# Kernel optimization log

Hardware: AMD Instinct MI355X
Metric: run time of the kernel (lower is better)

The kernel has to match this reference:

```python
import jax, jax.numpy as jnp
import numpy as np

N_SRC, N_DST, E = 50000, 50000, 800000
D_GT, D_AG = 64, 64
HID, HEADS = 256, 4
FPH = HID // HEADS  # 64
N_ACT = 16
NEG_SLOPE = 0.2  # DGL GATv2Conv default negative_slope


def setup_inputs() -> dict:
    key = jax.random.key(0)
    ks = jax.random.split(key, 16)
    f32 = jnp.float32
    return {
        "feat_gt": jax.random.normal(ks[0], (N_SRC, D_GT), f32),
        "feat_agent": jax.random.normal(ks[1], (N_DST, D_AG), f32),
        "h0": jax.random.normal(ks[2], (N_DST, HID), f32),
        "edge_src": jax.random.randint(ks[3], (E,), 0, N_SRC),
        "edge_dst": jax.random.randint(ks[4], (E,), 0, N_DST),
        "W_src": jax.random.normal(ks[5], (D_GT, HID), f32) * 0.1,
        "b_src": jnp.zeros((HID,), f32),
        "W_dst": jax.random.normal(ks[6], (D_AG, HID), f32) * 0.1,
        "b_dst": jnp.zeros((HID,), f32),
        "attn": jax.random.normal(ks[7], (HEADS, FPH), f32) * 0.1,
        "W_res": jax.random.normal(ks[8], (D_AG, HID), f32) * 0.1,
        "b_res": jnp.zeros((HID,), f32),
        "W_ih": jax.random.normal(ks[9], (3 * HID, HID), f32) * 0.05,
        "W_hh": jax.random.normal(ks[10], (3 * HID, HID), f32) * 0.05,
        "b_ih": jnp.zeros((3 * HID,), f32),
        "b_hh": jnp.zeros((3 * HID,), f32),
        "W_out": jax.random.normal(ks[11], (HID, N_ACT), f32) * 0.05,
        "b_out": jnp.zeros((N_ACT,), f32),
    }


def _gatv2(feat_gt, feat_agent, edge_src, edge_dst,
           W_src, b_src, W_dst, b_dst, attn, W_res, b_res):
    # GATv2Conv (bipartite, share_weights=False, residual=True, activation=ReLU)
    fs = (feat_gt @ W_src + b_src).reshape(N_SRC, HEADS, FPH)    # [Ns,H,F]
    fd = (feat_agent @ W_dst + b_dst).reshape(N_DST, HEADS, FPH)  # [Nd,H,F]
    e = fs[edge_src] + fd[edge_dst]                               # [E,H,F]
    e = jnp.where(e > 0, e, NEG_SLOPE * e)                        # LeakyReLU
    score = jnp.einsum('ehf,hf->eh', e, attn)                     # [E,H]
    # edge softmax segmented by destination node
    smax = jax.lax.stop_gradient(
        jax.ops.segment_max(score, edge_dst, num_segments=N_DST))  # [Nd,H]
    ex = jnp.exp(score - smax[edge_dst])
    den = jax.ops.segment_sum(ex, edge_dst, num_segments=N_DST)   # [Nd,H]
    alpha = ex / den[edge_dst]                                    # [E,H]
    msg = alpha[:, :, None] * fs[edge_src]                        # [E,H,F]
    rst = jax.ops.segment_sum(msg, edge_dst, num_segments=N_DST)  # [Nd,H,F]
    rst = rst.reshape(N_DST, HID) + (feat_agent @ W_res + b_res)  # residual
    return jax.nn.relu(rst)


def _gru_cell(x, h, W_ih, W_hh, b_ih, b_hh):
    gi = x @ W_ih.T + b_ih
    gh = h @ W_hh.T + b_hh
    ir, iz, inn = jnp.split(gi, 3, axis=-1)
    hr, hz, hn = jnp.split(gh, 3, axis=-1)
    r = jax.nn.sigmoid(ir + hr)
    z = jax.nn.sigmoid(iz + hz)
    n = jnp.tanh(inn + r * hn)
    return (1.0 - z) * n + z * h


def reference(feat_gt, feat_agent, h0, edge_src, edge_dst,
              W_src, b_src, W_dst, b_dst, attn, W_res, b_res,
              W_ih, W_hh, b_ih, b_hh, W_out, b_out):
    x = _gatv2(feat_gt, feat_agent, edge_src, edge_dst,
               W_src, b_src, W_dst, b_dst, attn, W_res, b_res)  # [Nd,HID]
    h = _gru_cell(x, h0, W_ih, W_hh, b_ih, b_hh)                # [Nd,HID]
    logits = h @ W_out + b_out                                  # [Nd,N_ACT]
    return (logits, h)
```

## Files before the change

kernel.cpp:

```cpp
#include <hip/hip_runtime.h>
#include <stdint.h>

#define N_SRCN 50000
#define N_DSTN 50000
#define NE     800000
#define HIDN   256
#define NEG    0.2f

typedef __attribute__((ext_vector_type(8)))  short short8;
typedef __attribute__((ext_vector_type(16))) float float16v;

__device__ __forceinline__ float bf2f(unsigned short u){
    union { unsigned u32; float f; } c; c.u32 = ((unsigned)u) << 16; return c.f;
}
__device__ __forceinline__ unsigned short f2bf(float f){
    union { float f; unsigned u; } c; c.f = f;
    unsigned r = c.u + 0x7fffu + ((c.u >> 16) & 1u);
    return (unsigned short)(r >> 16);
}
__device__ __forceinline__ float4 ld4b(const unsigned short* p){
    uint2 u = *reinterpret_cast<const uint2*>(p);
    float4 r;
    r.x = bf2f((unsigned short)(u.x & 0xffff));
    r.y = bf2f((unsigned short)(u.x >> 16));
    r.z = bf2f((unsigned short)(u.y & 0xffff));
    r.w = bf2f((unsigned short)(u.y >> 16));
    return r;
}
__device__ __forceinline__ void gload_lds16(const unsigned short* g, unsigned short* l){
    __builtin_amdgcn_global_load_lds(
        (const __attribute__((address_space(1))) void*)g,
        (__attribute__((address_space(3))) void*)l,
        16, 0, 0);
}

__global__ void pack_kernel(const float* __restrict__ Wsrc, const float* __restrict__ Wdst,
                            const float* __restrict__ Wres, const float* __restrict__ Wih,
                            const float* __restrict__ Whh,
                            unsigned short* __restrict__ Wt2,
                            unsigned short* __restrict__ Wf){
    int i = blockIdx.x * 256 + threadIdx.x;
    if (i < 49152){
        int which = i >> 14, j = i & 16383;
        int k = j >> 8, c = j & 255;
        const float* W = (which == 0) ? Wsrc : (which == 1 ? Wdst : Wres);
        float v = W[j];
        int off = which * 16384 + (c >> 5) * 2048 + (k >> 4) * 512
                + (((k >> 3) & 1) * 32 + (c & 31)) * 8 + (k & 7);
        Wt2[off] = f2bf(v);
    } else if (i < 49152 + 196608){
        int o = i - 49152;
        int row = o >> 8, k = o & 255;
        int g = row >> 8, c = row & 255;
        float v = Wih[o];
        int off = g * 131072 + (c >> 5) * 16384 + (k >> 4) * 512
                + (((k >> 3) & 1) * 32 + (c & 31)) * 8 + (k & 7);
        Wf[off] = f2bf(v);
    } else if (i < 49152 + 393216){
        int o = i - 49152 - 196608;
        int row = o >> 8, k = o & 255;
        int g = row >> 8, c = row & 255;
        float v = Whh[o];
        int off = g * 131072 + (c >> 5) * 16384 + (16 + (k >> 4)) * 512
                + (((k >> 3) & 1) * 32 + (c & 31)) * 8 + (k & 7);
        Wf[off] = f2bf(v);
    }
}

__global__ __launch_bounds__(256) void proj_kernel(
        const float* __restrict__ Agt, const float* __restrict__ Aag,
        const unsigned short* __restrict__ Wt2,
        const float* __restrict__ bsrc, const float* __restrict__ bdst,
        const float* __restrict__ bres,
        unsigned short* __restrict__ fs, unsigned short* __restrict__ fd,
        unsigned short* __restrict__ resb){
    __shared__ unsigned short As[64 * 72];
    __shared__ unsigned short Cs[64 * 72];
    int z = blockIdx.z;
    const float* A = (z == 0) ? Agt : Aag;
    const float* bias = (z == 0) ? bsrc : (z == 1 ? bdst : bres);
    unsigned short* out = (z == 0) ? fs : (z == 1 ? fd : resb);
    const unsigned short* Wb = Wt2 + z * 16384;
    int tid = threadIdx.x;
    int m0 = blockIdx.y * 64;
    #pragma unroll
    for (int i = 0; i < 4; ++i){
        int ci = tid + i * 256;
        int row = ci >> 4;
        int k4 = (ci & 15) << 2;
        int gr = m0 + row; if (gr >= N_SRCN) gr = N_SRCN - 1;
        float4 v = *reinterpret_cast<const float4*>(A + (size_t)gr * 64 + k4);
        unsigned short* dp = As + row * 72 + k4;
        dp[0] = f2bf(v.x); dp[1] = f2bf(v.y); dp[2] = f2bf(v.z); dp[3] = f2bf(v.w);
    }
    __syncthreads();
    int lane = tid & 63, w = tid >> 6;
    int l31 = lane & 31, half = lane >> 5;
    int msub = (w & 1) * 32;
    int cbw = blockIdx.x * 2 + (w >> 1);
    const unsigned short* bb = Wb + cbw * 2048 + lane * 8;
    const unsigned short* ap = As + (msub + l31) * 72 + half * 8;
    float16v acc = {0,0,0,0,0,0,0,0,0,0,0,0,0,0,0,0};
    #pragma unroll
    for (int ks = 0; ks < 4; ++ks){
        short8 a = *reinterpret_cast<const short8*>(ap + ks * 16);
        short8 b = *reinterpret_cast<const short8*>(bb + ks * 512);
        acc = __builtin_amdgcn_mfma_f32_32x32x16_bf16(a, b, acc, 0, 0, 0);
    }
    float bv = bias[cbw * 32 + l31];
    int ccol = (w >> 1) * 32 + l31;
    #pragma unroll
    for (int r = 0; r < 16; ++r){
        int row = (r & 3) + 8 * (r >> 2) + 4 * half + msub;
        Cs[row * 72 + ccol] = f2bf(acc[r] + bv);
    }
    __syncthreads();
    int srow = tid >> 2, chunk = tid & 3;
    int gr2 = m0 + srow;
    if (gr2 < N_SRCN){
        const uint4* sp = reinterpret_cast<const uint4*>(Cs + srow * 72 + chunk * 16);
        uint4* gp = reinterpret_cast<uint4*>(out + (size_t)gr2 * 256 + blockIdx.x * 64 + chunk * 16);
        gp[0] = sp[0];
        gp[1] = sp[1];
    }
}

__global__ void degree_kernel(const int* __restrict__ dst, int* __restrict__ deg){
    int i = blockIdx.x * 256 + threadIdx.x;
    if (i < NE) atomicAdd(&deg[dst[i]], 1);
}

__global__ void scan1_kernel(const int* __restrict__ deg, int* __restrict__ bsum){
    __shared__ int s[256];
    int tid = threadIdx.x;
    int i = blockIdx.x * 256 + tid;
    s[tid] = (i < N_DSTN) ? deg[i] : 0;
    __syncthreads();
    #pragma unroll
    for (int off = 128; off; off >>= 1){
        if (tid < off) s[tid] += s[tid + off];
        __syncthreads();
    }
    if (tid == 0) bsum[blockIdx.x] = s[0];
}

__global__ void scan2_kernel(const int* __restrict__ bsum, int* __restrict__ boff){
    __shared__ int s[256];
    int tid = threadIdx.x;
    int v = (tid < 196) ? bsum[tid] : 0;
    s[tid] = v;
    __syncthreads();
    #pragma unroll
    for (int off = 1; off < 256; off <<= 1){
        int t = (tid >= off) ? s[tid - off] : 0;
        __syncthreads();
        s[tid] += t;
        __syncthreads();
    }
    if (tid < 196) boff[tid] = s[tid] - v;
}

__global__ void scan3_kernel(const int* __restrict__ deg, const int* __restrict__ boff,
                             int* __restrict__ ptr, int* __restrict__ cursor){
    __shared__ int s[256];
    int tid = threadIdx.x;
    int i = blockIdx.x * 256 + tid;
    int v = (i < N_DSTN) ? deg[i] : 0;
    s[tid] = v;
    __syncthreads();
    #pragma unroll
    for (int off = 1; off < 256; off <<= 1){
        int t = (tid >= off) ? s[tid - off] : 0;
        __syncthreads();
        s[tid] += t;
        __syncthreads();
    }
    int ex = s[tid] - v + boff[blockIdx.x];
    if (i < N_DSTN){ ptr[i] = ex; cursor[i] = ex; }
}

__global__ void scatter_kernel(const int* __restrict__ src, const int* __restrict__ dst,
                               int* __restrict__ cursor, int* __restrict__ csr){
    int i = blockIdx.x * 256 + threadIdx.x;
    if (i < NE){
        int d = dst[i];
        int pos = atomicAdd(&cursor[d], 1);
        csr[pos] = src[i];
    }
}

__global__ __launch_bounds__(256) void aggregate_kernel(
        const unsigned short* __restrict__ fs, const unsigned short* __restrict__ fd,
        const unsigned short* __restrict__ res, const float* __restrict__ attn,
        const int* __restrict__ ptr, const int* __restrict__ deg,
        const int* __restrict__ csr, unsigned short* __restrict__ x){
    int wv = threadIdx.x >> 6;
    int d = blockIdx.x * 4 + wv;
    if (d >= N_DSTN) return;
    int lane = threadIdx.x & 63;
    int c4 = lane * 4;
    float4 fdv = ld4b(fd + (size_t)d * 256 + c4);
    float4 at = *reinterpret_cast<const float4*>(attn + (lane >> 4) * 64 + (lane & 15) * 4);
    int p = ptr[d], dg = deg[d];
    float l = 0.f;
    float4 acc = make_float4(0.f, 0.f, 0.f, 0.f);
    for (int base = 0; base < dg; base += 64){
        int cnt = min(64, dg - base);
        int sreg = (lane < cnt) ? csr[p + base + lane] : 0;
        float4 b0 = ld4b(fs + (size_t)__shfl(sreg, 0) * 256 + c4);
        float4 b1 = ld4b(fs + (size_t)__shfl(sreg, 1 & 63) * 256 + c4);
        float4 b2 = ld4b(fs + (size_t)__shfl(sreg, 2 & 63) * 256 + c4);
        float4 b3 = ld4b(fs + (size_t)__shfl(sreg, 3 & 63) * 256 + c4);
        for (int j = 0; j < cnt; j += 4){
            float4 n0 = ld4b(fs + (size_t)__shfl(sreg, (j + 4) & 63) * 256 + c4);
            float4 n1 = ld4b(fs + (size_t)__shfl(sreg, (j + 5) & 63) * 256 + c4);
            float4 n2 = ld4b(fs + (size_t)__shfl(sreg, (j + 6) & 63) * 256 + c4);
            float4 n3 = ld4b(fs + (size_t)__shfl(sreg, (j + 7) & 63) * 256 + c4);
#define PROC(BV, T) { \
            float ex = BV.x + fdv.x; ex = ex > 0.f ? ex : NEG * ex; \
            float ey = BV.y + fdv.y; ey = ey > 0.f ? ey : NEG * ey; \
            float ez = BV.z + fdv.z; ez = ez > 0.f ? ez : NEG * ez; \
            float ew = BV.w + fdv.w; ew = ew > 0.f ? ew : NEG * ew; \
            float part = ex * at.x + ey * at.y + ez * at.z + ew * at.w; \
            part += __shfl_xor(part, 1); \
            part += __shfl_xor(part, 2); \
            part += __shfl_xor(part, 4); \
            part += __shfl_xor(part, 8); \
            float wgt = ((j + (T)) < cnt) ? __expf(part) : 0.f; \
            l += wgt; \
            acc.x = fmaf(wgt, BV.x, acc.x); \
            acc.y = fmaf(wgt, BV.y, acc.y); \
            acc.z = fmaf(wgt, BV.z, acc.z); \
            acc.w = fmaf(wgt, BV.w, acc.w); }
            PROC(b0, 0) PROC(b1, 1) PROC(b2, 2) PROC(b3, 3)
#undef PROC
            b0 = n0; b1 = n1; b2 = n2; b3 = n3;
        }
    }
    float inv = (l > 0.f) ? 1.f / l : 0.f;
    float4 rv = ld4b(res + (size_t)d * 256 + c4);
    float xx = fmaxf(fmaf(acc.x, inv, rv.x), 0.f);
    float xy = fmaxf(fmaf(acc.y, inv, rv.y), 0.f);
    float xz = fmaxf(fmaf(acc.z, inv, rv.z), 0.f);
    float xw = fmaxf(fmaf(acc.w, inv, rv.w), 0.f);
    uint2 o;
    o.x = (unsigned)f2bf(xx) | ((unsigned)f2bf(xy) << 16);
    o.y = (unsigned)f2bf(xz) | ((unsigned)f2bf(xw) << 16);
    *reinterpret_cast<uint2*>(x + (size_t)d * 256 + c4) = o;
}

__global__ __launch_bounds__(1024, 4) void gru_kernel(
        const unsigned short* __restrict__ Xb,
        const float* __restrict__ H0, const unsigned short* __restrict__ Wf,
        const float* __restrict__ bih, const float* __restrict__ bhh,
        float* __restrict__ outH){
    __shared__ unsigned short As[64 * 512];
    __shared__ unsigned short Bs[2 * 12288];
    int tid = threadIdx.x;
    int m0 = blockIdx.x << 6;
    int w = tid >> 6, lane = tid & 63;
    #pragma unroll
    for (int i = 0; i < 2; ++i){
        int ci = tid + i * 1024;
        int row = ci >> 5, c = ci & 31;
        int gr = m0 + row; if (gr >= N_DSTN) gr = N_DSTN - 1;
        *reinterpret_cast<uint4*>(As + row * 512 + ((c ^ (row & 7)) << 3)) =
            *reinterpret_cast<const uint4*>(Xb + (size_t)gr * 256 + (c << 3));
    }
    #pragma unroll
    for (int i = 0; i < 2; ++i){
        int ci = tid + i * 1024;
        int row = ci >> 5, c = ci & 31;
        int gr = m0 + row; if (gr >= N_DSTN) gr = N_DSTN - 1;
        const float* hp = H0 + (size_t)gr * 256 + (c << 3);
        float4 f0 = *reinterpret_cast<const float4*>(hp);
        float4 f1 = *reinterpret_cast<const float4*>(hp + 4);
        uint4 o;
        o.x = (unsigned)f2bf(f0.x) | ((unsigned)f2bf(f0.y) << 16);
        o.y = (unsigned)f2bf(f0.z) | ((unsigned)f2bf(f0.w) << 16);
        o.z = (unsigned)f2bf(f1.x) | ((unsigned)f2bf(f1.y) << 16);
        o.w = (unsigned)f2bf(f1.z) | ((unsigned)f2bf(f1.w) << 16);
        *reinterpret_cast<uint4*>(As + row * 512 + (((c + 32) ^ (row & 7)) << 3)) = o;
    }
    {
        int g = w >> 3, cb = w & 7;
        gload_lds16(Wf + g * 131072 + cb * 16384 + lane * 8, Bs + w * 512);
        if (w < 8)
            gload_lds16(Wf + 2 * 131072 + w * 16384 + lane * 8, Bs + (16 + w) * 512);
    }
    __syncthreads();

    int l31 = lane & 31, half = lane >> 5;
    int rt = w >> 3, ct = w & 7;
    int arow = rt * 32 + l31;
    int rl = arow & 7;
    const unsigned short* apb = As + arow * 512;
    int sg = w >> 3, scb = w & 7;
    float16v zv = {0,0,0,0,0,0,0,0,0,0,0,0,0,0,0,0};
    float16v ar = zv, az = zv, anx = zv, anh = zv;
    #pragma unroll 2
    for (int p = 0; p < 32; ++p){
        if (p + 1 < 32){
            unsigned short* db = Bs + ((p + 1) & 1) * 12288;
            gload_lds16(Wf + sg * 131072 + scb * 16384 + (p + 1) * 512 + lane * 8,
                        db + w * 512);
            if (w < 8)
                gload_lds16(Wf + 2 * 131072 + w * 16384 + (p + 1) * 512 + lane * 8,
                            db + (16 + w) * 512);
        }
        const unsigned short* bp = Bs + (p & 1) * 12288;
        short8 a  = *reinterpret_cast<const short8*>(apb + (((p * 2 + half) ^ rl) << 3));
        short8 vr = *reinterpret_cast<const short8*>(bp + (0 * 8 + ct) * 512 + lane * 8);
        short8 vz = *reinterpret_cast<const short8*>(bp + (1 * 8 + ct) * 512 + lane * 8);
        short8 vn = *reinterpret_cast<const short8*>(bp + (2 * 8 + ct) * 512 + lane * 8);
        ar = __builtin_amdgcn_mfma_f32_32x32x16_bf16(a, vr, ar, 0, 0, 0);
        az = __builtin_amdgcn_mfma_f32_32x32x16_bf16(a, vz, az, 0, 0, 0);
        if (p < 16) anx = __builtin_amdgcn_mfma_f32_32x32x16_bf16(a, vn, anx, 0, 0, 0);
        else        anh = __builtin_amdgcn_mfma_f32_32x32x16_bf16(a, vn, anh, 0, 0, 0);
        __syncthreads();
    }
    int cg = ct * 32 + l31;
    float rb = bih[cg] + bhh[cg];
    float zb = bih[256 + cg] + bhh[256 + cg];
    float bin = bih[512 + cg], bhn = bhh[512 + cg];
    #pragma unroll
    for (int r = 0; r < 16; ++r){
        int m = m0 + rt * 32 + (r & 3) + 8 * (r >> 2) + 4 * half;
        if (m < N_DSTN){
            float h0v = H0[(size_t)m * 256 + cg];
            float rrg = 1.f / (1.f + __expf(-(ar[r] + rb)));
            float zg  = 1.f / (1.f + __expf(-(az[r] + zb)));
            float nx = anx[r] + bin + rrg * (anh[r] + bhn);
            float tm = __expf(-2.f * fabsf(nx));
            float nn = (1.f - tm) / (1.f + tm);
            nn = (nx >= 0.f) ? nn : -nn;
            outH[(size_t)m * 256 + cg] = (1.f - zg) * nn + zg * h0v;
        }
    }
}

__global__ __launch_bounds__(256) void logits_kernel(
        const float* __restrict__ H, const float* __restrict__ Wout,
        const float* __restrict__ bout, float* __restrict__ outL){
    __shared__ float Hl[16 * 260];
    __shared__ float Wl[16 * 260];
    int tid = threadIdx.x;
    int m0 = blockIdx.x * 16;
    #pragma unroll
    for (int i = 0; i < 4; ++i){
        int ci = tid + i * 256;
        int row = ci >> 6;
        int c4 = (ci & 63) << 2;
        int gr = m0 + row; if (gr >= N_DSTN) gr = N_DSTN - 1;
        float4 v = *reinterpret_cast<const float4*>(H + (size_t)gr * 256 + c4);
        float* dp = Hl + row * 260 + c4;
        dp[0] = v.x; dp[1] = v.y; dp[2] = v.z; dp[3] = v.w;
    }
    #pragma unroll
    for (int i = 0; i < 16; ++i){
        int ci = tid + i * 256;
        int c = ci >> 4, j = ci & 15;
        Wl[j * 260 + c] = Wout[c * 16 + j];
    }
    __syncthreads();
    int row = tid >> 4, j = tid & 15;
    const float* hr = Hl + row * 260;
    const float* wr = Wl + j * 260;
    float acc = bout[j];
    #pragma unroll
    for (int c = 0; c < 256; c += 4){
        float4 hv = *reinterpret_cast<const float4*>(hr + c);
        float4 wv = *reinterpret_cast<const float4*>(wr + c);
        acc = fmaf(hv.x, wv.x, fmaf(hv.y, wv.y, fmaf(hv.z, wv.z, fmaf(hv.w, wv.w, acc))));
    }
    int m = m0 + row;
    if (m < N_DSTN) outL[m * 16 + j] = acc;
}

extern "C" void kernel_launch(void* const* d_in, const int* in_sizes, int n_in,
                              void* d_out, int out_size, void* d_ws, size_t ws_size,
                              hipStream_t stream){
    const float* feat_gt = (const float*)d_in[0];
    const float* feat_ag = (const float*)d_in[1];
    const float* h0      = (const float*)d_in[2];
    const int*   e_src   = (const int*)d_in[3];
    const int*   e_dst   = (const int*)d_in[4];
    const float* W_src   = (const float*)d_in[5];
    const float* b_src   = (const float*)d_in[6];
    const float* W_dst   = (const float*)d_in[7];
    const float* b_dst   = (const float*)d_in[8];
    const float* attn    = (const float*)d_in[9];
    const float* W_res   = (const float*)d_in[10];
    const float* b_res   = (const float*)d_in[11];
    const float* W_ih    = (const float*)d_in[12];
    const float* W_hh    = (const float*)d_in[13];
    const float* b_ih    = (const float*)d_in[14];
    const float* b_hh    = (const float*)d_in[15];
    const float* W_out   = (const float*)d_in[16];
    const float* b_out   = (const float*)d_in[17];

    float* outL = (float*)d_out;
    float* outH = outL + (size_t)N_DSTN * 16;

    char* ws = (char*)d_ws;
    size_t off = 0;
    auto alloc = [&](size_t bytes) -> void* {
        void* p = ws + off; off = (off + bytes + 255) & ~(size_t)255; return p;
    };
    unsigned short* fs   = (unsigned short*)alloc((size_t)N_SRCN * 256 * 2);
    unsigned short* fd   = (unsigned short*)alloc((size_t)N_DSTN * 256 * 2);
    unsigned short* res  = (unsigned short*)alloc((size_t)N_DSTN * 256 * 2);
    unsigned short* xb   = (unsigned short*)alloc((size_t)N_DSTN * 256 * 2);
    unsigned short* Wt2  = (unsigned short*)alloc(49152 * 2);
    unsigned short* Wf   = (unsigned short*)alloc(393216 * 2);
    int* deg    = (int*)alloc(N_DSTN * 4);
    int* ptr    = (int*)alloc(N_DSTN * 4);
    int* cursor = (int*)alloc(N_DSTN * 4);
    int* csr    = (int*)alloc((size_t)NE * 4);
    int* bsum   = (int*)alloc(256 * 4);
    int* boff   = (int*)alloc(256 * 4);

    hipMemsetAsync(deg, 0, N_DSTN * 4, stream);
    pack_kernel<<<1728, 256, 0, stream>>>(W_src, W_dst, W_res, W_ih, W_hh, Wt2, Wf);

    proj_kernel<<<dim3(4, 782, 3), 256, 0, stream>>>(feat_gt, feat_ag, Wt2,
                                                     b_src, b_dst, b_res, fs, fd, res);

    degree_kernel<<<3125, 256, 0, stream>>>(e_dst, deg);
    scan1_kernel<<<196, 256, 0, stream>>>(deg, bsum);
    scan2_kernel<<<1, 256, 0, stream>>>(bsum, boff);
    scan3_kernel<<<196, 256, 0, stream>>>(deg, boff, ptr, cursor);
    scatter_kernel<<<3125, 256, 0, stream>>>(e_src, e_dst, cursor, csr);
    aggregate_kernel<<<12500, 256, 0, stream>>>(fs, fd, res, attn, ptr, deg, csr, xb);

    gru_kernel<<<782, 1024, 0, stream>>>(xb, h0, Wf, b_ih, b_hh, outH);
    logits_kernel<<<3125, 256, 0, stream>>>(outH, W_out, b_out, outL);
}
```

Measured before the change: 458.5 us.

## Triple-buffer GRU weight loads with manual vmcnt waits and single barrier

Reworks the GRU GEMM weight staging from a double buffer to a triple buffer with a prefetch distance of two. Loads are spread evenly over 12 waves, and explicit s_waitcnt plus one raw s_barrier per iteration replace the trailing __syncthreads. It also widens the LDS XOR swizzle for the A tile from 8 to 16 rows, fully unrolls the loop, and raises wave priority around the MFMAs. The aim is to hide global-to-LDS latency and cut barrier stalls, at the cost of extra LDS (which may lower occupancy) and fragile hand-counted vmcnt synchronisation.

After: 452.0 us. About the same (-1.4%).

```diff
diff --git a/kernel.cpp b/kernel.cpp
--- a/kernel.cpp
+++ b/kernel.cpp
@@ -255,7 +255,7 @@
         const float* __restrict__ bih, const float* __restrict__ bhh,
         float* __restrict__ outH){
     __shared__ unsigned short As[64 * 512];
-    __shared__ unsigned short Bs[2 * 12288];
+    __shared__ unsigned short Bs[3 * 12288];
     int tid = threadIdx.x;
     int m0 = blockIdx.x << 6;
     int w = tid >> 6, lane = tid & 63;
@@ -264,7 +264,7 @@
         int ci = tid + i * 1024;
         int row = ci >> 5, c = ci & 31;
         int gr = m0 + row; if (gr >= N_DSTN) gr = N_DSTN - 1;
-        *reinterpret_cast<uint4*>(As + row * 512 + ((c ^ (row & 7)) << 3)) =
+        *reinterpret_cast<uint4*>(As + row * 512 + ((c ^ (row & 15)) << 3)) =
             *reinterpret_cast<const uint4*>(Xb + (size_t)gr * 256 + (c << 3));
     }
     #pragma unroll
@@ -280,44 +280,51 @@
         o.y = (unsigned)f2bf(f0.z) | ((unsigned)f2bf(f0.w) << 16);
         o.z = (unsigned)f2bf(f1.x) | ((unsigned)f2bf(f1.y) << 16);
         o.w = (unsigned)f2bf(f1.z) | ((unsigned)f2bf(f1.w) << 16);
-        *reinterpret_cast<uint4*>(As + row * 512 + (((c + 32) ^ (row & 7)) << 3)) = o;
-    }
-    {
-        int g = w >> 3, cb = w & 7;
-        gload_lds16(Wf + g * 131072 + cb * 16384 + lane * 8, Bs + w * 512);
-        if (w < 8)
-            gload_lds16(Wf + 2 * 131072 + w * 16384 + lane * 8, Bs + (16 + w) * 512);
-    }
-    __syncthreads();
+        *reinterpret_cast<uint4*>(As + row * 512 + (((c + 32) ^ (row & 15)) << 3)) = o;
+    }
+    __syncthreads();
+
+    int s0 = 2 * w, s1 = 2 * w + 1;
+    const unsigned short* g0 = Wf + (s0 >> 3) * 131072 + (s0 & 7) * 16384 + lane * 8;
+    const unsigned short* g1 = Wf + (s1 >> 3) * 131072 + (s1 & 7) * 16384 + lane * 8;
+    if (w < 12){
+        gload_lds16(g0,       Bs + s0 * 512);
+        gload_lds16(g1,       Bs + s1 * 512);
+        gload_lds16(g0 + 512, Bs + 12288 + s0 * 512);
+        gload_lds16(g1 + 512, Bs + 12288 + s1 * 512);
+    }
 
     int l31 = lane & 31, half = lane >> 5;
     int rt = w >> 3, ct = w & 7;
     int arow = rt * 32 + l31;
-    int rl = arow & 7;
+    int rl = arow & 15;
     const unsigned short* apb = As + arow * 512;
-    int sg = w >> 3, scb = w & 7;
     float16v zv = {0,0,0,0,0,0,0,0,0,0,0,0,0,0,0,0};
     float16v ar = zv, az = zv, anx = zv, anh = zv;
-    #pragma unroll 2
+    #pragma unroll
     for (int p = 0; p < 32; ++p){
-        if (p + 1 < 32){
-            unsigned short* db = Bs + ((p + 1) & 1) * 12288;
-            gload_lds16(Wf + sg * 131072 + scb * 16384 + (p + 1) * 512 + lane * 8,
-                        db + w * 512);
-            if (w < 8)
-                gload_lds16(Wf + 2 * 131072 + w * 16384 + (p + 1) * 512 + lane * 8,
-                            db + (16 + w) * 512);
+        if (w < 12){
+            if (p >= 31) asm volatile("s_waitcnt vmcnt(0)" ::: "memory");
+            else         asm volatile("s_waitcnt vmcnt(2)" ::: "memory");
         }
-        const unsigned short* bp = Bs + (p & 1) * 12288;
+        __builtin_amdgcn_s_barrier();
+        __builtin_amdgcn_sched_barrier(0);
+        if (p + 2 < 32 && w < 12){
+            unsigned short* db = Bs + ((p + 2) % 3) * 12288;
+            gload_lds16(g0 + (p + 2) * 512, db + s0 * 512);
+            gload_lds16(g1 + (p + 2) * 512, db + s1 * 512);
+        }
+        const unsigned short* bp = Bs + (p % 3) * 12288;
         short8 a  = *reinterpret_cast<const short8*>(apb + (((p * 2 + half) ^ rl) << 3));
         short8 vr = *reinterpret_cast<const short8*>(bp + (0 * 8 + ct) * 512 + lane * 8);
         short8 vz = *reinterpret_cast<const short8*>(bp + (1 * 8 + ct) * 512 + lane * 8);
         short8 vn = *reinterpret_cast<const short8*>(bp + (2 * 8 + ct) * 512 + lane * 8);
+        __builtin_amdgcn_s_setprio(1);
         ar = __builtin_amdgcn_mfma_f32_32x32x16_bf16(a, vr, ar, 0, 0, 0);
         az = __builtin_amdgcn_mfma_f32_32x32x16_bf16(a, vz, az, 0, 0, 0);
         if (p < 16) anx = __builtin_amdgcn_mfma_f32_32x32x16_bf16(a, vn, anx, 0, 0, 0);
         else        anh = __builtin_amdgcn_mfma_f32_32x32x16_bf16(a, vn, anh, 0, 0, 0);
-        __syncthreads();
+        __builtin_amdgcn_s_setprio(0);
     }
     int cg = ct * 32 + l31;
     float rb = bih[cg] + bhh[cg];
```
